# Kernel tuning notes

Hardware: AMD Instinct MI355X
Metric: run time of the kernel (lower is better)

## Reference

```python
import jax, jax.numpy as jnp
import numpy as np

H = 1024

def _cell(xt, h, c, Wi, bi, Wh, bh):
    # gates: [B, 4H], torch Linear is x @ W.T + b; gate order i,f,g,o
    gates = xt @ Wi.T + bi + h @ Wh.T + bh
    i, f, g, o = jnp.split(gates, 4, axis=1)
    i = jax.nn.sigmoid(i)
    f = jax.nn.sigmoid(f)
    g = jnp.tanh(g)
    o = jax.nn.sigmoid(o)
    c_next = f * c + i * g
    h_next = o * jnp.tanh(c_next)
    return h_next, c_next

def setup_inputs() -> dict:
    key = jax.random.key(0)
    ks = jax.random.split(key, 12)
    vocab, E, out_dim = 32000, 1024, 32000
    B, T = 32, 512
    std = 1.0 / np.sqrt(H)
    u = lambda k, shape: jax.random.uniform(k, shape, jnp.float32, -std, std)
    return {
        "x": jax.random.randint(ks[0], (B, T), 0, vocab, dtype=jnp.int32),
        "emb": jax.random.normal(ks[1], (vocab, E), jnp.float32),
        "Wi0": u(ks[2], (4 * H, E)),  "bi0": u(ks[3], (4 * H,)),
        "Wh0": u(ks[4], (4 * H, H)), "bh0": u(ks[5], (4 * H,)),
        "Wi1": u(ks[6], (4 * H, H)), "bi1": u(ks[7], (4 * H,)),
        "Wh1": u(ks[8], (4 * H, H)), "bh1": u(ks[9], (4 * H,)),
        "fc_w": u(ks[10], (out_dim, H)) * (std * np.sqrt(H)) / np.sqrt(H),
        "fc_b": u(ks[11], (out_dim,)),
    }

def reference(x, emb, Wi0, bi0, Wh0, bh0, Wi1, bi1, Wh1, bh1, fc_w, fc_b):
    B, T = x.shape
    xe = emb[x]  # [B, T, E]
    xe = jnp.transpose(xe, (1, 0, 2))  # [T, B, E]
    init = (jnp.zeros((B, H), xe.dtype), jnp.zeros((B, H), xe.dtype),
            jnp.zeros((B, H), xe.dtype), jnp.zeros((B, H), xe.dtype))

    def step(carry, xt):
        h0, c0, h1, c1 = carry
        h0, c0 = _cell(xt, h0, c0, Wi0, bi0, Wh0, bh0)
        h1, c1 = _cell(h0, h1, c1, Wi1, bi1, Wh1, bh1)
        return (h0, c0, h1, c1), None

    (h0, c0, h1, c1), _ = jax.lax.scan(step, init, xe)
    return h1 @ fc_w.T + fc_b  # [B, out_dim]
```

## Files before the change

### kernel.cpp

```cpp
#include <hip/hip_runtime.h>
#include <hip/hip_bf16.h>

typedef __attribute__((ext_vector_type(8))) short short8;
typedef __attribute__((ext_vector_type(4))) float f32x4;
typedef __attribute__((ext_vector_type(4))) int i32x4;
typedef unsigned short u16;
typedef unsigned int u32;
typedef unsigned long long u64;

#define MFMA_BF16(a, b, c) __builtin_amdgcn_mfma_f32_16x16x32_bf16((a), (b), (c), 0, 0, 0)

static constexpr size_t OFF_W   = 0;
static constexpr size_t OFF_B0  = 33554432;
static constexpr size_t OFF_B1  = OFF_B0 + 16384;
static constexpr size_t OFF_H0  = OFF_B1 + 16384;
static constexpr size_t OFF_H1F = OFF_H0 + 262144;
static constexpr size_t OFF_XE  = OFF_H1F + 131072;
static constexpr size_t OFF_X0  = OFF_XE + 33554432;
static constexpr size_t WS_NEED = OFF_X0 + 134217728;
static constexpr size_t OFF_FLG = OFF_X0 - 4096;


__device__ __forceinline__ u16 f2bf(float f) {
  u32 x = __builtin_bit_cast(u32, f);
  x += 0x7fffu + ((x >> 16) & 1u);
  return (u16)(x >> 16);
}
__device__ __forceinline__ float bf2f(u16 u) {
  return __builtin_bit_cast(float, (u32)u << 16);
}

__device__ __forceinline__ float fexp2(float x) {
  float r; asm("v_exp_f32 %0, %1" : "=v"(r) : "v"(x)); return r;
}
__device__ __forceinline__ float frcp(float x) {
  float r; asm("v_rcp_f32 %0, %1" : "=v"(r) : "v"(x)); return r;
}
__device__ __forceinline__ float sigm(float x) {
  return frcp(1.f + fexp2(-1.44269504f * x));
}
__device__ __forceinline__ float ftanh(float x) {
  float xc = fminf(fmaxf(x, -15.f), 15.f);
  float e = fexp2(2.88539008f * xc);
  return (e - 1.f) * frcp(e + 1.f);
}

__device__ __forceinline__ void sysstore64(void* p, u64 v) {
  __hip_atomic_store((u64*)p, v, __ATOMIC_RELAXED, __HIP_MEMORY_SCOPE_SYSTEM);
}
__device__ __forceinline__ u64 sysload64(const void* p) {
  return __hip_atomic_load((const u64*)p, __ATOMIC_RELAXED, __HIP_MEMORY_SCOPE_SYSTEM);
}

__device__ __forceinline__ void gload_lds16(const u16* gsrc, u16* ldst) {
  __builtin_amdgcn_global_load_lds(
      (__attribute__((address_space(1))) void*)(u16*)gsrc,
      (__attribute__((address_space(3))) void*)ldst, 16, 0, 0);
}

__global__ void prep_w_kernel(const float* __restrict__ Wi0, const float* __restrict__ Wh0,
                              const float* __restrict__ Wi1, const float* __restrict__ Wh1,
                              u16* __restrict__ dst) {
  size_t e = ((size_t)blockIdx.x * 256 + threadIdx.x) * 4;
  int mat = (int)(e >> 22);
  size_t off = e & ((1ull << 22) - 1);
  const float* src = (mat == 0) ? Wi0 : (mat == 1) ? Wh0 : (mat == 2) ? Wi1 : Wh1;
  float4 v = *(const float4*)(src + off);
  ushort4 o;
  o.x = f2bf(v.x); o.y = f2bf(v.y); o.z = f2bf(v.z); o.w = f2bf(v.w);
  *(ushort4*)(dst + e) = o;
}

__global__ void prep_b_kernel(const float* __restrict__ bi0, const float* __restrict__ bh0,
                              const float* __restrict__ bi1, const float* __restrict__ bh1,
                              float* __restrict__ b0, float* __restrict__ b1) {
  int i = blockIdx.x * 256 + threadIdx.x;
  b0[i] = bi0[i] + bh0[i];
  b1[i] = bi1[i] + bh1[i];
}

__global__ void embed_kernel(const int* __restrict__ x, const float* __restrict__ emb,
                             u16* __restrict__ xe) {
  int m = blockIdx.x;
  int b = m & 31, t = m >> 5;
  int id = x[b * 512 + t];
  float4 v = ((const float4*)(emb + (size_t)id * 1024))[threadIdx.x];
  ushort4 o;
  o.x = f2bf(v.x); o.y = f2bf(v.y); o.z = f2bf(v.z); o.w = f2bf(v.w);
  *(ushort4*)(xe + (size_t)m * 1024 + threadIdx.x * 4) = o;
}

__global__ void x0_gemm_kernel(const u16* __restrict__ A, const u16* __restrict__ W,
                               const float* __restrict__ bias, u16* __restrict__ Xp) {
  __shared__ u16 lds[2][2][8192];
  const int tid = threadIdx.x, l = tid & 63, w = tid >> 6;
  const int n0 = blockIdx.x * 128, m0 = blockIdx.y * 128;
  const int wm = w >> 1, wn = w & 1;
  const int row8 = l >> 3, u = l & 7;

  f32x4 acc[4][4];
#pragma unroll
  for (int a1 = 0; a1 < 4; ++a1)
#pragma unroll
    for (int a2 = 0; a2 < 4; ++a2) acc[a1][a2] = (f32x4){0.f, 0.f, 0.f, 0.f};

  auto stage = [&](int buf, int kt) {
    const int k0 = kt * 64;
#pragma unroll
    for (int q = 0; q < 4; ++q) {
      const int ld = w * 4 + q;
      const int row = ld * 8 + row8;
      const int sw = (u ^ (row & 7)) * 8;
      gload_lds16(A + (size_t)(m0 + row) * 1024 + k0 + sw, &lds[buf][0][ld * 512]);
      gload_lds16(W + (size_t)(n0 + row) * 1024 + k0 + sw, &lds[buf][1][ld * 512]);
    }
  };

  stage(0, 0);
  __syncthreads();

  for (int kt = 0; kt < 16; ++kt) {
    const int buf = kt & 1;
    if (kt < 15) stage(buf ^ 1, kt + 1);
    const u16* la = lds[buf][0];
    const u16* lb = lds[buf][1];
#pragma unroll
    for (int kk = 0; kk < 2; ++kk) {
      const int c = kk * 4 + (l >> 4);
      const int csw = (c ^ (l & 7)) * 8;
      short8 af[4], bf[4];
#pragma unroll
      for (int mi = 0; mi < 4; ++mi) {
        int row = wm * 64 + mi * 16 + (l & 15);
        af[mi] = *(const short8*)(la + row * 64 + csw);
      }
#pragma unroll
      for (int ni = 0; ni < 4; ++ni) {
        int row = wn * 64 + ni * 16 + (l & 15);
        bf[ni] = *(const short8*)(lb + row * 64 + csw);
      }
#pragma unroll
      for (int mi = 0; mi < 4; ++mi)
#pragma unroll
        for (int ni = 0; ni < 4; ++ni)
          acc[mi][ni] = MFMA_BF16(af[mi], bf[ni], acc[mi][ni]);
    }
    __syncthreads();
  }

#pragma unroll
  for (int ni = 0; ni < 4; ++ni) {
    int col = n0 + wn * 64 + ni * 16 + (l & 15);
    int g = col >> 10, blkid = (col & 1023) >> 2, j = col & 3;
    float bv = bias[col];
#pragma unroll
    for (int mi = 0; mi < 4; ++mi) {
#pragma unroll
      for (int r = 0; r < 4; ++r) {
        int row = m0 + wm * 64 + mi * 16 + (l >> 4) * 4 + r;
        int t = row >> 5, b = row & 31;
        Xp[(size_t)t * 131072 + blkid * 512 + b * 16 + j * 4 + g] =
            f2bf(acc[mi][ni][r] + bv);
      }
    }
  }
}

__launch_bounds__(256, 1)
__global__ void lstm_kernel(const u16* __restrict__ wbf, const float* __restrict__ b1v,
                            const u16* __restrict__ Xp, u16* __restrict__ hinit,
                            float* __restrict__ h1f, u32* __restrict__ flagsD) {
  extern __shared__ char smem[];
  u16* wlds = (u16*)smem;
  float* gates0 = (float*)(smem + 98304);
  float* part1  = (float*)(smem + 98304 + 2048);
  float* wh1p   = (float*)(smem + 98304 + 4096);

  const int tid = threadIdx.x;
  const int l = tid & 63, w = tid >> 6;
  const int blk = blockIdx.x;
  const int hbase = blk * 4;
  u16* Xw = (u16*)Xp;

  for (int m = 0; m < 3; ++m) {
    const u16* Wm = wbf + (size_t)(m + 1) * (4096 * 1024);
    for (int s = tid; s < 2048; s += 256) {
      int kk = s >> 6, ll = s & 63;
      int nl = ll & 15, hi = ll >> 4;
      int gr = (nl >> 2) * 1024 + hbase + (nl & 3);
      short8 v = *(const short8*)(Wm + (size_t)gr * 1024 + kk * 32 + hi * 8);
      *(short8*)(wlds + m * 16384 + kk * 512 + ll * 8) = v;
    }
  }
  __syncthreads();

  float cst = 0.f;
  const int at = tid & 127, ab = at >> 2, aj = at & 3;
  const int mt = w & 1;

  float b1i = 0.f, b1fv = 0.f, b1g = 0.f, b1o = 0.f;
  if (tid >= 128) {
    b1i  = b1v[hbase + aj];
    b1fv = b1v[1024 + hbase + aj];
    b1g  = b1v[2048 + hbase + aj];
    b1o  = b1v[3072 + hbase + aj];
  }

  u64 gchunk = 0;
  if (tid < 128)
    gchunk = sysload64(Xp + blk * 512 + ab * 16 + aj * 4);

  const u32* fquad = flagsD + l * 4;

  for (int i = 0; i <= 512; ++i) {
    const u16* slot_r = (i == 0) ? hinit
                      : (i == 1) ? hinit + 65536
                                 : Xp + (size_t)(i - 2) * 131072;
    u16* slot_w = (i == 0) ? hinit + 65536
                           : Xw + (size_t)(i - 1) * 131072;

    asm volatile("" ::: "memory");

    const u16* abase = slot_r + (w < 2 ? 0 : 32768)
                     + (mt * 16 + (l & 15)) * 1024 + ((l >> 4) * 8);
    short8 ar[32];
#pragma unroll
    for (int kk = 0; kk < 32; ++kk)
      ar[kk] = *(const short8*)(abase + kk * 32);

    if (w < 2) {
      f32x4 a0a = {0,0,0,0}, a0b = {0,0,0,0}, a1a = {0,0,0,0}, a1b = {0,0,0,0};
#pragma unroll
      for (int kk = 0; kk < 16; ++kk) {
        a0a = MFMA_BF16(ar[2 * kk],     *(const short8*)(wlds + (2 * kk) * 512 + l * 8), a0a);
        a1a = MFMA_BF16(ar[2 * kk],     *(const short8*)(wlds + 16384 + (2 * kk) * 512 + l * 8), a1a);
        a0b = MFMA_BF16(ar[2 * kk + 1], *(const short8*)(wlds + (2 * kk + 1) * 512 + l * 8), a0b);
        a1b = MFMA_BF16(ar[2 * kk + 1], *(const short8*)(wlds + 16384 + (2 * kk + 1) * 512 + l * 8), a1b);
      }
#pragma unroll
      for (int r = 0; r < 4; ++r) {
        int row = mt * 16 + (l >> 4) * 4 + r, col = l & 15;
        gates0[row * 16 + col] = a0a[r] + a0b[r];
        part1[row * 16 + col]  = a1a[r] + a1b[r];
      }
    } else {
      f32x4 a0a = {0,0,0,0}, a0b = {0,0,0,0};
#pragma unroll
      for (int kk = 0; kk < 16; ++kk) {
        a0a = MFMA_BF16(ar[2 * kk],     *(const short8*)(wlds + 2 * 16384 + (2 * kk) * 512 + l * 8), a0a);
        a0b = MFMA_BF16(ar[2 * kk + 1], *(const short8*)(wlds + 2 * 16384 + (2 * kk + 1) * 512 + l * 8), a0b);
      }
#pragma unroll
      for (int r = 0; r < 4; ++r) {
        int row = mt * 16 + (l >> 4) * 4 + r, col = l & 15;
        wh1p[row * 16 + col] = a0a[r] + a0b[r];
      }
    }
    __syncthreads();

    if (tid < 128) {
      if (i < 512) {
        float gi = gates0[ab * 16 + aj]      + bf2f((u16)(gchunk));
        float gf = gates0[ab * 16 + 4 + aj]  + bf2f((u16)(gchunk >> 16));
        float gg = gates0[ab * 16 + 8 + aj]  + bf2f((u16)(gchunk >> 32));
        float go = gates0[ab * 16 + 12 + aj] + bf2f((u16)(gchunk >> 48));
        cst = sigm(gf) * cst + sigm(gi) * ftanh(gg);
        float h = sigm(go) * ftanh(cst);
        u32 hv = (u32)f2bf(h);
        u32 p1 = (u32)__shfl_xor((int)hv, 1);
        u32 lo = (aj & 1) ? ((p1 & 0xffff) | (hv << 16)) : ((hv & 0xffff) | (p1 << 16));
        u32 p2 = (u32)__shfl_xor((int)lo, 2);
        if (aj == 0)
          sysstore64(slot_w + ab * 1024 + hbase, (u64)lo | ((u64)p2 << 32));
      }
    } else {
      if (i >= 1) {
        float gi = part1[ab * 16 + aj]      + wh1p[ab * 16 + aj]      + b1i;
        float gf = part1[ab * 16 + 4 + aj]  + wh1p[ab * 16 + 4 + aj]  + b1fv;
        float gg = part1[ab * 16 + 8 + aj]  + wh1p[ab * 16 + 8 + aj]  + b1g;
        float go = part1[ab * 16 + 12 + aj] + wh1p[ab * 16 + 12 + aj] + b1o;
        cst = sigm(gf) * cst + sigm(gi) * ftanh(gg);
        float h = sigm(go) * ftanh(cst);
        u32 hv = (u32)f2bf(h);
        u32 p1 = (u32)__shfl_xor((int)hv, 1);
        u32 lo = (aj & 1) ? ((p1 & 0xffff) | (hv << 16)) : ((hv & 0xffff) | (p1 << 16));
        u32 p2 = (u32)__shfl_xor((int)lo, 2);
        if (aj == 0)
          sysstore64(slot_w + 32768 + ab * 1024 + hbase, (u64)lo | ((u64)p2 << 32));
        if (i == 512) h1f[ab * 1024 + hbase + aj] = h;
      }
    }

    if (i == 512) break;

    __syncthreads();
    const u32 target = (u32)(i + 1);
    if (tid == 0)
      __hip_atomic_store(&flagsD[blk], target, __ATOMIC_RELAXED, __HIP_MEMORY_SCOPE_SYSTEM);

    if (tid < 128 && i + 1 < 512)
      gchunk = sysload64(Xp + (size_t)(i + 1) * 131072 + blk * 512 + ab * 16 + aj * 4);

    if (w == 0) {
      while (true) {
        i32x4 v;
        asm volatile("global_load_dwordx4 %0, %1, off sc0 sc1"
                     : "=&v"(v) : "v"(fquad));
        asm volatile("s_waitcnt vmcnt(0)" ::: "memory");
        u32 m01 = min((u32)v.x, (u32)v.y);
        u32 m23 = min((u32)v.z, (u32)v.w);
        if (__all(min(m01, m23) >= target)) break;
      }
    }
    __syncthreads();
  }
}

__global__ void __launch_bounds__(512) fc_kernel(const float* __restrict__ h1f,
                                                 const float* __restrict__ fcw,
                                                 const float* __restrict__ fcb,
                                                 float* __restrict__ out) {
  extern __shared__ float hls[];
  for (int s = threadIdx.x; s < 8192; s += 512)
    ((float4*)hls)[s] = ((const float4*)h1f)[s];
  __syncthreads();
  const int w = threadIdx.x >> 6, l = threadIdx.x & 63;
  const int vbase = blockIdx.x * 128 + w * 16;
  for (int vi = 0; vi < 16; ++vi) {
    const int v = vbase + vi;
    const float4* wr = (const float4*)(fcw + (size_t)v * 1024);
    float4 f0 = wr[l], f1 = wr[64 + l], f2 = wr[128 + l], f3 = wr[192 + l];
    float bias = fcb[v];
    for (int b = 0; b < 32; ++b) {
      const float4* hb = (const float4*)(hls + b * 1024);
      float4 h0 = hb[l], h1 = hb[64 + l], h2 = hb[128 + l], h3 = hb[192 + l];
      float s = f0.x*h0.x + f0.y*h0.y + f0.z*h0.z + f0.w*h0.w
              + f1.x*h1.x + f1.y*h1.y + f1.z*h1.z + f1.w*h1.w
              + f2.x*h2.x + f2.y*h2.y + f2.z*h2.z + f2.w*h2.w
              + f3.x*h3.x + f3.y*h3.y + f3.z*h3.z + f3.w*h3.w;
      s += __shfl_xor(s, 1);  s += __shfl_xor(s, 2);  s += __shfl_xor(s, 4);
      s += __shfl_xor(s, 8);  s += __shfl_xor(s, 16); s += __shfl_xor(s, 32);
      if (l == 0) out[(size_t)b * 32000 + v] = s + bias;
    }
  }
}

extern "C" void kernel_launch(void* const* d_in, const int* in_sizes, int n_in,
                              void* d_out, int out_size, void* d_ws, size_t ws_size,
                              hipStream_t stream) {
  const int*   x   = (const int*)d_in[0];
  const float* emb = (const float*)d_in[1];
  const float* Wi0 = (const float*)d_in[2];
  const float* bi0 = (const float*)d_in[3];
  const float* Wh0 = (const float*)d_in[4];
  const float* bh0 = (const float*)d_in[5];
  const float* Wi1 = (const float*)d_in[6];
  const float* bi1 = (const float*)d_in[7];
  const float* Wh1 = (const float*)d_in[8];
  const float* bh1 = (const float*)d_in[9];
  const float* fcw = (const float*)d_in[10];
  const float* fcb = (const float*)d_in[11];
  float* out = (float*)d_out;
  char* ws = (char*)d_ws;

  if (ws_size < WS_NEED) return;

  u16*   wbf = (u16*)(ws + OFF_W);
  float* b0v = (float*)(ws + OFF_B0);
  float* b1v = (float*)(ws + OFF_B1);
  u16*   hin = (u16*)(ws + OFF_H0);
  float* h1f = (float*)(ws + OFF_H1F);
  u16*   xe  = (u16*)(ws + OFF_XE);
  u16*   Xp  = (u16*)(ws + OFF_X0);
  u32*   flg = (u32*)(ws + OFF_FLG);

  hipMemsetAsync(ws + OFF_H0, 0, OFF_XE - OFF_H0, stream);

  prep_w_kernel<<<16384, 256, 0, stream>>>(Wi0, Wh0, Wi1, Wh1, wbf);
  prep_b_kernel<<<16, 256, 0, stream>>>(bi0, bh0, bi1, bh1, b0v, b1v);
  embed_kernel<<<16384, 256, 0, stream>>>(x, emb, xe);
  x0_gemm_kernel<<<dim3(32, 128), 256, 0, stream>>>(xe, wbf, b0v, Xp);

  hipMemsetAsync(ws + OFF_FLG, 0, 4096, stream);

  hipFuncSetAttribute((const void*)lstm_kernel,
                      hipFuncAttributeMaxDynamicSharedMemorySize, 104448);
  lstm_kernel<<<256, 256, 104448, stream>>>(wbf, b1v, Xp, hin, h1f, flg);

  hipFuncSetAttribute((const void*)fc_kernel,
                      hipFuncAttributeMaxDynamicSharedMemorySize, 131072);
  fc_kernel<<<250, 512, 131072, stream>>>(h1f, fcw, fcb, out);
}
```

Baseline: 3.439 ms.

## Enlarge x0 GEMM tile to 256x128 with 8 waves and explicit prefetch pipeline

The input-projection GEMM now uses 512-thread blocks that each cover 256 rows, so every loaded W tile is reused across more rows. Global-to-LDS loads are staged two k-tiles ahead, and the per-iteration __syncthreads is replaced by an explicit s_waitcnt vmcnt plus s_barrier so loads overlap compute. This needs 96KB of dynamic LDS and limits occupancy to one block per CU. It only affects the pre-LSTM GEMM, which is likely a small part of total time next to the sequential LSTM kernel.

```diff
diff --git a/kernel.cpp b/kernel.cpp
--- a/kernel.cpp
+++ b/kernel.cpp
@@ -90,11 +90,15 @@
   *(ushort4*)(xe + (size_t)m * 1024 + threadIdx.x * 4) = o;
 }
 
+__launch_bounds__(512, 1)
 __global__ void x0_gemm_kernel(const u16* __restrict__ A, const u16* __restrict__ W,
                                const float* __restrict__ bias, u16* __restrict__ Xp) {
-  __shared__ u16 lds[2][2][8192];
+  extern __shared__ u16 lds[];
+  u16* ldsA = lds;
+  u16* ldsB = lds + 32768;
+
   const int tid = threadIdx.x, l = tid & 63, w = tid >> 6;
-  const int n0 = blockIdx.x * 128, m0 = blockIdx.y * 128;
+  const int n0 = blockIdx.x * 128, m0 = blockIdx.y * 256;
   const int wm = w >> 1, wn = w & 1;
   const int row8 = l >> 3, u = l & 7;
 
@@ -110,20 +114,30 @@
     for (int q = 0; q < 4; ++q) {
       const int ld = w * 4 + q;
       const int row = ld * 8 + row8;
-      const int sw = (u ^ (row & 7)) * 8;
-      gload_lds16(A + (size_t)(m0 + row) * 1024 + k0 + sw, &lds[buf][0][ld * 512]);
-      gload_lds16(W + (size_t)(n0 + row) * 1024 + k0 + sw, &lds[buf][1][ld * 512]);
+      const int sw = (u ^ row8) * 8;
+      gload_lds16(A + (size_t)(m0 + row) * 1024 + k0 + sw, ldsA + buf * 16384 + ld * 512);
+    }
+#pragma unroll
+    for (int q = 0; q < 2; ++q) {
+      const int ld = w * 2 + q;
+      const int row = ld * 8 + row8;
+      const int sw = (u ^ row8) * 8;
+      gload_lds16(W + (size_t)(n0 + row) * 1024 + k0 + sw, ldsB + buf * 8192 + ld * 512);
     }
   };
 
   stage(0, 0);
-  __syncthreads();
+  stage(1, 1);
 
   for (int kt = 0; kt < 16; ++kt) {
-    const int buf = kt & 1;
-    if (kt < 15) stage(buf ^ 1, kt + 1);
-    const u16* la = lds[buf][0];
-    const u16* lb = lds[buf][1];
+    const int cur = kt & 1;
+    if (kt < 14) asm volatile("s_waitcnt vmcnt(6)" ::: "memory");
+    else         asm volatile("s_waitcnt vmcnt(0)" ::: "memory");
+    __builtin_amdgcn_s_barrier();
+    __builtin_amdgcn_sched_barrier(0);
+
+    const u16* la = ldsA + cur * 16384;
+    const u16* lb = ldsB + cur * 8192;
 #pragma unroll
     for (int kk = 0; kk < 2; ++kk) {
       const int c = kk * 4 + (l >> 4);
@@ -145,7 +159,12 @@
         for (int ni = 0; ni < 4; ++ni)
           acc[mi][ni] = MFMA_BF16(af[mi], bf[ni], acc[mi][ni]);
     }
-    __syncthreads();
+
+    if (kt < 14) {
+      __builtin_amdgcn_s_barrier();
+      __builtin_amdgcn_sched_barrier(0);
+      stage(cur, kt + 2);
+    }
   }
 
 #pragma unroll
@@ -379,7 +398,10 @@
   prep_w_kernel<<<16384, 256, 0, stream>>>(Wi0, Wh0, Wi1, Wh1, wbf);
   prep_b_kernel<<<16, 256, 0, stream>>>(bi0, bh0, bi1, bh1, b0v, b1v);
   embed_kernel<<<16384, 256, 0, stream>>>(x, emb, xe);
-  x0_gemm_kernel<<<dim3(32, 128), 256, 0, stream>>>(xe, wbf, b0v, Xp);
+
+  hipFuncSetAttribute((const void*)x0_gemm_kernel,
+                      hipFuncAttributeMaxDynamicSharedMemorySize, 98304);
+  x0_gemm_kernel<<<dim3(32, 64), 512, 98304, stream>>>(xe, wbf, b0v, Xp);
 
   hipMemsetAsync(ws + OFF_FLG, 0, 4096, stream);
 
```

After: 3.431 ms, median of 2. About the same (-0.2%).
